# Kernel optimization log

Measured on AMD Instinct MI355X. Metric: run time of the kernel, lower is better.

The kernel has to match this reference:

```python
import jax, jax.numpy as jnp
import numpy as np

B, N = 1, 512
CS, CZ = 384, 128
H, DQK, DV, PQK, PV = 12, 16, 16, 4, 8
EPS = 1e-8
SW = float(np.sqrt(1.0 / (3 * DQK)))            # scalar_weights
PW = float(np.sqrt(1.0 / (3 * PQK * 9.0 / 2)))  # point_weights
ZW = float(np.sqrt(1.0 / 3))                    # attention_2d_weights


def _lin(key, din, dout):
    return 0.02 * jax.random.normal(key, (din, dout), dtype=jnp.float32), jnp.zeros((dout,), dtype=jnp.float32)


def setup_inputs():
    key = jax.random.key(0)
    ks = jax.random.split(key, 16)
    Wsq, bsq = _lin(ks[0], CS, H * DQK)
    Wsk, bsk = _lin(ks[1], CS, H * DQK)
    Wsv, bsv = _lin(ks[2], CS, H * DV)
    Wsb, bsb = _lin(ks[3], CZ, H)
    Wpq, bpq = _lin(ks[4], CS, H * PQK * 3)
    Wpk, bpk = _lin(ks[5], CS, H * PQK * 3)
    Wpv, bpv = _lin(ks[6], CS, H * PV * 3)
    Wout, bout = _lin(ks[7], H * (DV + PV * 4 + CZ), CS)
    w_attn = 0.5 * jax.random.normal(ks[8], (3,), dtype=jnp.float32)  # attn_linear weight (1,3)
    b_attn = jnp.zeros((), dtype=jnp.float32)
    tpw = jnp.full((H,), float(np.log(np.e - 1.0)), dtype=jnp.float32)  # trainable_point_weight
    s = jax.random.normal(ks[9], (B, N, CS), dtype=jnp.float32)
    z = jax.random.normal(ks[10], (B, N, N, CZ), dtype=jnp.float32)
    rot = jax.random.normal(ks[11], (B, N, 3, 3), dtype=jnp.float32)
    tran = jax.random.normal(ks[12], (B, N, 3), dtype=jnp.float32)
    res_mask = jnp.ones((B, N), dtype=jnp.float32)
    return dict(s=s, z=z, rot=rot, tran=tran, res_mask=res_mask,
                Wsq=Wsq, bsq=bsq, Wsk=Wsk, bsk=bsk, Wsv=Wsv, bsv=bsv,
                Wsb=Wsb, bsb=bsb, Wpq=Wpq, bpq=bpq, Wpk=Wpk, bpk=bpk,
                Wpv=Wpv, bpv=bpv, w_attn=w_attn, b_attn=b_attn, tpw=tpw,
                Wout=Wout, bout=bout)


def _ipa(s, z, rot, tran, res_mask, Wsq, bsq, Wsk, bsk, Wsv, bsv, Wsb, bsb,
         Wpq, bpq, Wpk, bpk, Wpv, bpv, w_attn, b_attn, tpw, Wout, bout):
    b, n, _ = s.shape
    sq = (s @ Wsq + bsq).reshape(b, n, H, DQK)
    sk = (s @ Wsk + bsk).reshape(b, n, H, DQK)
    sv = (s @ Wsv + bsv).reshape(b, n, H, DV)
    sb = z @ Wsb + bsb  # [b, i, j, h] pair bias

    def to_global(W, bias, p):
        t = (s @ W + bias).reshape(b, n, H, p, 3)
        return jnp.einsum('bnxy,bnhpy->bnhpx', rot, t) + tran[:, :, None, None, :]

    pqg = to_global(Wpq, bpq, PQK)
    pkg = to_global(Wpk, bpk, PQK)
    pvg = to_global(Wpv, bpv, PV)

    diff = pqg[:, :, None] - pkg[:, None, :]          # [b, i, j, h, p, 3]
    sdist = jnp.sum(diff * diff, axis=(-1, -2))       # [b, i, j, h]

    attn_point = -0.5 * jax.nn.softplus(tpw) * sdist * PW
    attn_scalar = jnp.einsum('bihd,bjhd->bijh', sq * SW, sk)
    attn_pair = sb * ZW
    # attn_linear(stack([scalar, point, pair], -1)).squeeze(-1)
    logits = attn_scalar * w_attn[0] + attn_point * w_attn[1] + attn_pair * w_attn[2] + b_attn

    mask2d = res_mask[:, :, None] * res_mask[:, None, :]
    logits = jnp.where(mask2d[..., None] == 0, jnp.finfo(logits.dtype).min, logits)
    attn = jax.nn.softmax(logits, axis=2)             # softmax over j

    r_scalar = jnp.einsum('bijh,bjhd->bihd', attn, sv)
    r_pt_g = jnp.einsum('bijh,bjhpc->bihpc', attn, pvg)
    # rotate back to local frame: R^T (x - t)
    r_pt = jnp.einsum('biyx,bihpy->bihpx', rot, r_pt_g - tran[:, :, None, None, :])
    r_norm = jnp.sqrt(jnp.sum(r_pt * r_pt, axis=-1) + EPS)  # [b, i, h, p]
    r_pair = jnp.einsum('bijh,bijc->bihc', attn, z)

    cat = jnp.concatenate([r_scalar, r_pt.reshape(b, n, H, PV * 3), r_norm, r_pair], axis=-1)
    return cat.reshape(b, n, -1) @ Wout + bout


def reference(s, z, rot, tran, res_mask, Wsq, bsq, Wsk, bsk, Wsv, bsv, Wsb, bsb,
              Wpq, bpq, Wpk, bpk, Wpv, bpv, w_attn, b_attn, tpw, Wout, bout):
    return _ipa(s, z, rot, tran, res_mask, Wsq, bsq, Wsk, bsk, Wsv, bsv, Wsb, bsb,
                Wpq, bpq, Wpk, bpk, Wpv, bpv, w_attn, b_attn, tpw, Wout, bout)
```

## Files before the change

### kernel.cpp

```cpp
#include <hip/hip_runtime.h>
#include <hip/hip_bf16.h>
#include <math.h>

#define NN 512
#define CSD 384
#define CZ 128
#define HH 12
#define TMPW 1152
#define CATH 176
#define CATDIM 2112
#define NSPLIT 6
#define KSPL 352

#define SW 0.14433756729740643f
#define PW 0.13608276348795434f
#define ZW 0.57735026918962576f
#define NEG_INF -3.4028234663852886e38f

typedef float f32x4_t __attribute__((ext_vector_type(4)));
typedef short bf16x8_t __attribute__((ext_vector_type(8)));

union BFU { uint4 q; bf16x8_t v; ushort u[8]; };

static __device__ __forceinline__ ushort f2bf(float f) {
    __hip_bfloat16 h = __float2bfloat16(f);
    return *reinterpret_cast<ushort*>(&h);
}
static __device__ __forceinline__ float bf2f(ushort u) {
    unsigned int v = ((unsigned int)u) << 16;
    return __uint_as_float(v);
}

__global__ void proj_gemm_kernel(const float* __restrict__ s, const float* __restrict__ rot,
                                 const float* __restrict__ tran,
                                 const float* __restrict__ Wsq, const float* __restrict__ bsq,
                                 const float* __restrict__ Wsk, const float* __restrict__ bsk,
                                 const float* __restrict__ Wsv, const float* __restrict__ bsv,
                                 const float* __restrict__ Wpq, const float* __restrict__ bpq,
                                 const float* __restrict__ Wpk, const float* __restrict__ bpk,
                                 const float* __restrict__ Wpv, const float* __restrict__ bpv,
                                 float* __restrict__ tmp)
{
    int bx = blockIdx.x;
    int n0 = blockIdx.y * 32;
    int f0 = bx * 48;
    const float* W; const float* bb; int dout; int segstart;
    if (bx < 4)       { W = Wsq; bb = bsq; dout = 192; segstart = 0; }
    else if (bx < 8)  { W = Wsk; bb = bsk; dout = 192; segstart = 192; }
    else if (bx < 12) { W = Wsv; bb = bsv; dout = 192; segstart = 384; }
    else if (bx < 15) { W = Wpq; bb = bpq; dout = 144; segstart = 576; }
    else if (bx < 18) { W = Wpk; bb = bpk; dout = 144; segstart = 720; }
    else              { W = Wpv; bb = bpv; dout = 288; segstart = 864; }
    int colbase = f0 - segstart;

    __shared__ float St[32][34];
    __shared__ float Ws[32][49];
    int tid = threadIdx.x;
    int ty = tid >> 4, tx = tid & 15;
    float acc[2][3] = {{0,0,0},{0,0,0}};

    for (int k0 = 0; k0 < CSD; k0 += 32) {
        {
            int r = tid >> 3, c4 = (tid & 7) * 4;
            float4 v = *(const float4*)&s[(size_t)(n0 + r) * CSD + k0 + c4];
            St[c4 + 0][r] = v.x; St[c4 + 1][r] = v.y; St[c4 + 2][r] = v.z; St[c4 + 3][r] = v.w;
        }
        for (int e = tid; e < 1536; e += 256) {
            int r = e / 48, c = e % 48;
            Ws[r][c] = W[(size_t)(k0 + r) * dout + colbase + c];
        }
        __syncthreads();
        #pragma unroll
        for (int k = 0; k < 32; k++) {
            float2 a = *(const float2*)&St[k][ty * 2];
            float b0 = Ws[k][tx * 3], b1 = Ws[k][tx * 3 + 1], b2 = Ws[k][tx * 3 + 2];
            acc[0][0] += a.x * b0; acc[0][1] += a.x * b1; acc[0][2] += a.x * b2;
            acc[1][0] += a.y * b0; acc[1][1] += a.y * b1; acc[1][2] += a.y * b2;
        }
        __syncthreads();
    }
    float bv0 = bb[colbase + tx * 3], bv1 = bb[colbase + tx * 3 + 1], bv2 = bb[colbase + tx * 3 + 2];
    #pragma unroll
    for (int r = 0; r < 2; r++) {
        int n = n0 + ty * 2 + r;
        float v0 = acc[r][0] + bv0, v1 = acc[r][1] + bv1, v2 = acc[r][2] + bv2;
        float* o = tmp + (size_t)n * TMPW + f0 + tx * 3;
        if (bx >= 12) {
            const float* R = rot + n * 9;
            const float* T = tran + n * 3;
            float g0 = R[0] * v0 + R[1] * v1 + R[2] * v2 + T[0];
            float g1 = R[3] * v0 + R[4] * v1 + R[5] * v2 + T[1];
            float g2 = R[6] * v0 + R[7] * v1 + R[8] * v2 + T[2];
            o[0] = g0; o[1] = g1; o[2] = g2;
        } else {
            o[0] = v0; o[1] = v1; o[2] = v2;
        }
    }
}

__global__ __launch_bounds__(256) void logits_kernel(
        const float* __restrict__ z, const float* __restrict__ resm,
        const float* __restrict__ Wsb, const float* __restrict__ bsb,
        const float* __restrict__ watt, const float* __restrict__ batt,
        const float* __restrict__ tpw, const float* __restrict__ tmp,
        float* __restrict__ lgts)
{
    int jc = blockIdx.x;
    int i  = blockIdx.y;
    __shared__ float sqs[12 * 24];
    __shared__ float pqi[12 * 24];
    __shared__ float cpt[12];
    __shared__ float cb[12];
    int tid = threadIdx.x;
    int w = tid >> 6, lane = tid & 63;
    int l16 = lane & 15, lhi = lane >> 4;
    float w0 = watt[0], w1 = watt[1], w2 = watt[2], ba = batt[0];
    float A2 = w2 * ZW;

    if (tid < 192) {
        int h = tid >> 4, d = tid & 15;
        sqs[h * 24 + d] = tmp[(size_t)i * TMPW + tid] * (SW * w0);
    }
    if (tid < 144) {
        int h = tid / 12, d = tid % 12;
        pqi[h * 24 + d] = tmp[(size_t)i * TMPW + 576 + tid];
    }
    if (tid < 12) {
        cpt[tid] = -0.5f * log1pf(expf(tpw[tid])) * PW * w1;
        cb[tid]  = A2 * bsb[tid] + ba;
    }

    BFU breg[4];
    #pragma unroll
    for (int kk = 0; kk < 4; kk++) {
        #pragma unroll
        for (int e = 0; e < 8; e++) {
            int k = kk * 32 + lhi * 8 + e;
            float v = (l16 < HH) ? Wsb[k * HH + l16] * A2 : 0.f;
            breg[kk].u[e] = f2bf(v);
        }
    }
    __syncthreads();

    const float* zi = z + (size_t)i * NN * CZ;
    float rmi = resm[i];
    float cpth = cpt[l16 < HH ? l16 : 0];
    float cbh  = cb[l16 < HH ? l16 : 0];

    #pragma unroll
    for (int t = 0; t < 2; t++) {
        int jbase = jc * 128 + (w * 2 + t) * 16;
        const float* zr = zi + (size_t)(jbase + l16) * CZ + lhi * 8;
        float4 pr[8];
        #pragma unroll
        for (int kk = 0; kk < 4; kk++) {
            pr[kk * 2]     = *(const float4*)&zr[kk * 32];
            pr[kk * 2 + 1] = *(const float4*)&zr[kk * 32 + 4];
        }
        f32x4_t acc = {0.f, 0.f, 0.f, 0.f};
        #pragma unroll
        for (int kk = 0; kk < 4; kk++) {
            float4 f0 = pr[kk * 2], f1 = pr[kk * 2 + 1];
            BFU a;
            a.u[0] = f2bf(f0.x); a.u[1] = f2bf(f0.y); a.u[2] = f2bf(f0.z); a.u[3] = f2bf(f0.w);
            a.u[4] = f2bf(f1.x); a.u[5] = f2bf(f1.y); a.u[6] = f2bf(f1.z); a.u[7] = f2bf(f1.w);
            acc = __builtin_amdgcn_mfma_f32_16x16x32_bf16(a.v, breg[kk].v, acc, 0, 0, 0);
        }
        if (l16 < HH) {
            int h = l16;
            const float4* sqp = (const float4*)&sqs[h * 24];
            const float4* pqp = (const float4*)&pqi[h * 24];
            #pragma unroll
            for (int r = 0; r < 4; r++) {
                int j = jbase + lhi * 4 + r;
                float mj = rmi * resm[j];
                const float4* skp = (const float4*)(tmp + (size_t)j * TMPW + 192 + h * 16);
                float d0 = 0.f;
                #pragma unroll
                for (int q = 0; q < 4; q++) {
                    float4 kv = skp[q];
                    float4 qv = sqp[q];
                    d0 += qv.x * kv.x + qv.y * kv.y + qv.z * kv.z + qv.w * kv.w;
                }
                const float4* pkp = (const float4*)(tmp + (size_t)j * TMPW + 720 + h * 12);
                float sd = 0.f;
                #pragma unroll
                for (int q = 0; q < 3; q++) {
                    float4 kv = pkp[q];
                    float4 qv = pqp[q];
                    float a = qv.x - kv.x, bb2 = qv.y - kv.y, cc = qv.z - kv.z, e = qv.w - kv.w;
                    sd += a * a + bb2 * bb2 + cc * cc + e * e;
                }
                float lg = cbh + acc[r] + d0 + cpth * sd;
                if (mj == 0.f) lg = NEG_INF;
                lgts[((size_t)i * HH + h) * NN + j] = lg;
            }
        }
    }
}

__global__ __launch_bounds__(256) void softmax_kernel(const float* __restrict__ lgts,
                                                      ushort* __restrict__ attn_bf)
{
    int tid = threadIdx.x;
    int w = tid >> 6, lane = tid & 63;
    int gid = blockIdx.x * 4 + w;
    const float* row = lgts + (size_t)gid * NN;
    float v[8]; float m = -INFINITY;
    #pragma unroll
    for (int u = 0; u < 8; u++) { v[u] = row[lane + 64 * u]; m = fmaxf(m, v[u]); }
    for (int off = 32; off; off >>= 1) m = fmaxf(m, __shfl_xor(m, off));
    float ssum = 0.f;
    #pragma unroll
    for (int u = 0; u < 8; u++) { v[u] = __expf(v[u] - m); ssum += v[u]; }
    for (int off = 32; off; off >>= 1) ssum += __shfl_xor(ssum, off);
    float inv = 1.f / ssum;
    ushort* ag = attn_bf + (size_t)gid * NN;
    #pragma unroll
    for (int u = 0; u < 8; u++) ag[lane + 64 * u] = f2bf(v[u] * inv);
}

__global__ __launch_bounds__(256) void rpair_kernel(const float* __restrict__ z,
                                                    const ushort* __restrict__ attn_bf,
                                                    float* __restrict__ part)
{
    int jq = blockIdx.x;
    int i  = blockIdx.y;
    __shared__ ushort pbf[128 * 12];
    __shared__ float pslab[4 * 12 * 128];
    int tid = threadIdx.x;

    if (tid < 192) {
        int h = tid >> 4, g = tid & 15;
        BFU v; v.q = *(const uint4*)&attn_bf[((size_t)i * HH + h) * NN + jq * 128 + g * 8];
        #pragma unroll
        for (int q = 0; q < 8; q++) pbf[(g * 8 + q) * 12 + h] = v.u[q];
    }
    __syncthreads();

    int w = tid >> 6, lane = tid & 63;
    int c0 = lane * 2;
    const float* zq = z + ((size_t)i * NN + jq * 128 + w * 32) * CZ + c0;
    float acc[12][2];
    #pragma unroll
    for (int h = 0; h < 12; h++) { acc[h][0] = 0.f; acc[h][1] = 0.f; }

    for (int j0 = 0; j0 < 32; j0 += 8) {
        float2 zv[8];
        #pragma unroll
        for (int u = 0; u < 8; u++) zv[u] = *(const float2*)&zq[(size_t)(j0 + u) * CZ];
        #pragma unroll
        for (int u = 0; u < 8; u++) {
            int jl = w * 32 + j0 + u;
            const uint2* pr = (const uint2*)&pbf[jl * 12];
            uint2 pa = pr[0], pb2 = pr[1], pc = pr[2];
            float ph[12];
            ph[0]  = bf2f((ushort)(pa.x & 0xffff)); ph[1]  = bf2f((ushort)(pa.x >> 16));
            ph[2]  = bf2f((ushort)(pa.y & 0xffff)); ph[3]  = bf2f((ushort)(pa.y >> 16));
            ph[4]  = bf2f((ushort)(pb2.x & 0xffff)); ph[5]  = bf2f((ushort)(pb2.x >> 16));
            ph[6]  = bf2f((ushort)(pb2.y & 0xffff)); ph[7]  = bf2f((ushort)(pb2.y >> 16));
            ph[8]  = bf2f((ushort)(pc.x & 0xffff)); ph[9]  = bf2f((ushort)(pc.x >> 16));
            ph[10] = bf2f((ushort)(pc.y & 0xffff)); ph[11] = bf2f((ushort)(pc.y >> 16));
            #pragma unroll
            for (int h = 0; h < 12; h++) {
                acc[h][0] += ph[h] * zv[u].x;
                acc[h][1] += ph[h] * zv[u].y;
            }
        }
    }
    #pragma unroll
    for (int h = 0; h < 12; h++)
        *(float2*)&pslab[(w * 12 + h) * 128 + c0] = make_float2(acc[h][0], acc[h][1]);
    __syncthreads();

    for (int e = tid; e < 1536; e += 256) {
        float ssum = pslab[e] + pslab[1536 + e] + pslab[3072 + e] + pslab[4608 + e];
        part[((size_t)jq * NN + i) * 1536 + e] = ssum;
    }
}

__global__ void combine_rpair_kernel(const float* __restrict__ part, float* __restrict__ cat)
{
    int v = blockIdx.x * 256 + threadIdx.x;
    int i = v / 1536, hc = v % 1536;
    int h = hc >> 7, c = hc & 127;
    float ssum = part[(size_t)i * 1536 + hc]
               + part[((size_t)NN + i) * 1536 + hc]
               + part[((size_t)2 * NN + i) * 1536 + hc]
               + part[((size_t)3 * NN + i) * 1536 + hc];
    cat[(size_t)i * CATDIM + h * CATH + 48 + c] = ssum;
}

__global__ void head_sum_kernel(const ushort* __restrict__ attn_bf, const float* __restrict__ tmp,
                                const float* __restrict__ rot, const float* __restrict__ tran,
                                float* __restrict__ cat)
{
    int i0 = blockIdx.x * 32;
    int h  = blockIdx.y;
    __shared__ float At[32][65];
    __shared__ float Sr[64][44];
    __shared__ float Rp[32][24];
    int tid = threadIdx.x;
    int il = tid & 31, fg = tid >> 5;
    float acc[5] = {0,0,0,0,0};

    for (int jc = 0; jc < NN; jc += 64) {
        {
            int r = tid >> 3, c8 = (tid & 7) * 8;
            const ushort* src = attn_bf + ((size_t)(i0 + r) * HH + h) * NN + jc + c8;
            BFU v; v.q = *(const uint4*)src;
            #pragma unroll
            for (int q = 0; q < 8; q++) At[r][c8 + q] = bf2f(v.u[q]);
        }
        {
            int jr = tid >> 2, d4 = (tid & 3) * 4;
            *(float4*)&Sr[jr][d4] = *(const float4*)&tmp[(size_t)(jc + jr) * TMPW + 384 + h * 16 + d4];
        }
        for (int e = tid; e < 384; e += 256) {
            int jr = e / 6, p4 = (e % 6) * 4;
            *(float4*)&Sr[jr][16 + p4] = *(const float4*)&tmp[(size_t)(jc + jr) * TMPW + 864 + h * 24 + p4];
        }
        __syncthreads();
        #pragma unroll 4
        for (int j = 0; j < 64; j++) {
            float a = At[il][j];
            #pragma unroll
            for (int q = 0; q < 5; q++) acc[q] += a * Sr[j][fg * 5 + q];
        }
        __syncthreads();
    }

    float* cbase = cat + (size_t)(i0 + il) * CATDIM + h * CATH;
    #pragma unroll
    for (int q = 0; q < 5; q++) {
        int f = fg * 5 + q;
        if (f < 16) cbase[f] = acc[q];
        else Rp[il][f - 16] = acc[q];
    }
    __syncthreads();

    {
        int il2 = tid >> 3, p = tid & 7;
        int i = i0 + il2;
        float gx = Rp[il2][p * 3 + 0] - tran[i * 3 + 0];
        float gy = Rp[il2][p * 3 + 1] - tran[i * 3 + 1];
        float gz = Rp[il2][p * 3 + 2] - tran[i * 3 + 2];
        const float* R = rot + i * 9;
        float lx = R[0] * gx + R[3] * gy + R[6] * gz;
        float ly = R[1] * gx + R[4] * gy + R[7] * gz;
        float lz = R[2] * gx + R[5] * gy + R[8] * gz;
        float nrm = sqrtf(lx * lx + ly * ly + lz * lz + 1e-8f);
        float* cp = cat + (size_t)i * CATDIM + h * CATH;
        cp[16 + p * 3 + 0] = lx; cp[16 + p * 3 + 1] = ly; cp[16 + p * 3 + 2] = lz;
        cp[40 + p] = nrm;
    }
}

__global__ void out_gemm_split_kernel(const float* __restrict__ cat, const float* __restrict__ Wout,
                                      float* __restrict__ part)
{
    int n0 = blockIdx.x * 64;
    int i0 = blockIdx.y * 64;
    int ks = blockIdx.z * KSPL;
    __shared__ float St[32][68];
    __shared__ float Bs[32][68];
    int tid = threadIdx.x;
    int ty = tid >> 4, tx = tid & 15;
    float acc[4][4] = {{0,0,0,0},{0,0,0,0},{0,0,0,0},{0,0,0,0}};

    for (int k0 = 0; k0 < KSPL; k0 += 32) {
        {
            int r = tid >> 2, c8 = (tid & 3) * 8;
            const float* src = cat + (size_t)(i0 + r) * CATDIM + ks + k0 + c8;
            float4 v0 = *(const float4*)src;
            float4 v1 = *(const float4*)(src + 4);
            St[c8+0][r]=v0.x; St[c8+1][r]=v0.y; St[c8+2][r]=v0.z; St[c8+3][r]=v0.w;
            St[c8+4][r]=v1.x; St[c8+5][r]=v1.y; St[c8+6][r]=v1.z; St[c8+7][r]=v1.w;
        }
        {
            int r = tid >> 3, c8 = (tid & 7) * 8;
            const float* src = Wout + (size_t)(ks + k0 + r) * CSD + n0 + c8;
            *(float4*)&Bs[r][c8]     = *(const float4*)src;
            *(float4*)&Bs[r][c8 + 4] = *(const float4*)(src + 4);
        }
        __syncthreads();
        #pragma unroll
        for (int k = 0; k < 32; k++) {
            float4 a = *(const float4*)&St[k][ty * 4];
            float4 b = *(const float4*)&Bs[k][tx * 4];
            float av[4] = {a.x, a.y, a.z, a.w};
            float bv[4] = {b.x, b.y, b.z, b.w};
            #pragma unroll
            for (int r = 0; r < 4; r++)
                #pragma unroll
                for (int c = 0; c < 4; c++) acc[r][c] += av[r] * bv[c];
        }
        __syncthreads();
    }
    #pragma unroll
    for (int r = 0; r < 4; r++) {
        float4 v = make_float4(acc[r][0], acc[r][1], acc[r][2], acc[r][3]);
        *(float4*)&part[((size_t)blockIdx.z * NN + i0 + ty * 4 + r) * CSD + n0 + tx * 4] = v;
    }
}

__global__ void reduce_out_kernel(const float* __restrict__ part, const float* __restrict__ bout,
                                  float* __restrict__ out)
{
    int v = blockIdx.x * 256 + threadIdx.x;
    int n4 = v % 96;
    float4 o = ((const float4*)bout)[n4];
    const float4* p4 = (const float4*)part;
    #pragma unroll
    for (int s = 0; s < NSPLIT; s++) {
        float4 t = p4[(size_t)s * 49152 + v];
        o.x += t.x; o.y += t.y; o.z += t.z; o.w += t.w;
    }
    ((float4*)out)[v] = o;
}

extern "C" void kernel_launch(void* const* d_in, const int* in_sizes, int n_in,
                              void* d_out, int out_size, void* d_ws, size_t ws_size,
                              hipStream_t stream) {
    const float* s    = (const float*)d_in[0];
    const float* z    = (const float*)d_in[1];
    const float* rot  = (const float*)d_in[2];
    const float* tran = (const float*)d_in[3];
    const float* resm = (const float*)d_in[4];
    const float* Wsq  = (const float*)d_in[5];  const float* bsq = (const float*)d_in[6];
    const float* Wsk  = (const float*)d_in[7];  const float* bsk = (const float*)d_in[8];
    const float* Wsv  = (const float*)d_in[9];  const float* bsv = (const float*)d_in[10];
    const float* Wsb  = (const float*)d_in[11]; const float* bsb = (const float*)d_in[12];
    const float* Wpq  = (const float*)d_in[13]; const float* bpq = (const float*)d_in[14];
    const float* Wpk  = (const float*)d_in[15]; const float* bpk = (const float*)d_in[16];
    const float* Wpv  = (const float*)d_in[17]; const float* bpv = (const float*)d_in[18];
    const float* watt = (const float*)d_in[19]; const float* batt = (const float*)d_in[20];
    const float* tpw  = (const float*)d_in[21];
    const float* Wout = (const float*)d_in[22]; const float* bout = (const float*)d_in[23];
    float* out = (float*)d_out;
    float* ws  = (float*)d_ws;

    float*  tmp     = ws;
    ushort* attn_bf = (ushort*)(ws + 589824);
    float*  lgts    = ws + 589824 + 1572864;
    float*  partR   = lgts + 3145728;
    float*  cat     = partR + 3145728;
    float*  partO   = cat + 1081344;

    proj_gemm_kernel<<<dim3(24, 16), 256, 0, stream>>>(s, rot, tran,
                                                       Wsq, bsq, Wsk, bsk, Wsv, bsv,
                                                       Wpq, bpq, Wpk, bpk, Wpv, bpv, tmp);
    logits_kernel<<<dim3(4, 512), 256, 0, stream>>>(z, resm, Wsb, bsb, watt, batt,
                                                    tpw, tmp, lgts);
    softmax_kernel<<<1536, 256, 0, stream>>>(lgts, attn_bf);
    rpair_kernel<<<dim3(4, 512), 256, 0, stream>>>(z, attn_bf, partR);
    combine_rpair_kernel<<<3072, 256, 0, stream>>>(partR, cat);
    head_sum_kernel<<<dim3(16, 12), 256, 0, stream>>>(attn_bf, tmp, rot, tran, cat);
    out_gemm_split_kernel<<<dim3(6, 8, NSPLIT), 256, 0, stream>>>(cat, Wout, partO);
    reduce_out_kernel<<<192, 256, 0, stream>>>(partO, bout, out);
}
```

Before: 200.5 us.

## Compute scalar and point logits as augmented bf16 MFMA GEMM fused into softmax

The squared point distance is expanded algebraically into q·k plus norm terms, so the scalar, point and bias logit contributions become one 32-wide augmented dot product. A prep kernel builds bf16 Q/K augmented matrices, and the softmax kernel computes the 16x512 tile per head with MFMA before adding the z-derived logits. The z-logits kernel now only does the pair-bias MFMA, dropping the per-element fp32 gathers from tmp. The rpair loop is also unrolled to 16 z loads in flight. Rounding the operands to bf16 and cancellation in the expanded distance (|q|²+|k|²-2q·k) can reduce logit accuracy, and the change adds one extra launch.

```diff
diff --git a/kernel.cpp b/kernel.cpp
--- a/kernel.cpp
+++ b/kernel.cpp
@@ -98,37 +98,66 @@
     }
 }
 
-__global__ __launch_bounds__(256) void logits_kernel(
-        const float* __restrict__ z, const float* __restrict__ resm,
-        const float* __restrict__ Wsb, const float* __restrict__ bsb,
-        const float* __restrict__ watt, const float* __restrict__ batt,
-        const float* __restrict__ tpw, const float* __restrict__ tmp,
-        float* __restrict__ lgts)
+__global__ void augprep_kernel(const float* __restrict__ tmp,
+                               const float* __restrict__ watt, const float* __restrict__ batt,
+                               const float* __restrict__ tpw, const float* __restrict__ bsb,
+                               ushort* __restrict__ Qaug, ushort* __restrict__ Kaug)
+{
+    int n = blockIdx.x;
+    int tid = threadIdx.x;
+    float w0 = watt[0], w1 = watt[1], w2 = watt[2], ba = batt[0];
+    float A2 = w2 * ZW;
+    __shared__ float nq[12], nk[12];
+    if (tid < 24) {
+        int h = tid >> 1, which = tid & 1;
+        const float* p = tmp + (size_t)n * TMPW + (which ? 720 : 576) + h * 12;
+        float s2 = 0.f;
+        #pragma unroll
+        for (int d = 0; d < 12; d++) s2 += p[d] * p[d];
+        if (which) nk[h] = s2; else nq[h] = s2;
+    }
+    __syncthreads();
+
+    for (int f = tid; f < 384; f += 256) {
+        if (f < 192) {
+            int h = f >> 4, k = f & 15;
+            float sq = tmp[(size_t)n * TMPW + h * 16 + k] * (SW * w0);
+            float sk = tmp[(size_t)n * TMPW + 192 + h * 16 + k];
+            Qaug[((size_t)h * NN + n) * 32 + k] = f2bf(sq);
+            Kaug[((size_t)h * NN + n) * 32 + k] = f2bf(sk);
+        } else if (f < 336) {
+            int e = f - 192; int h = e / 12, d = e % 12;
+            float cpt = -0.5f * log1pf(expf(tpw[h])) * PW * w1;
+            float pq = tmp[(size_t)n * TMPW + 576 + h * 12 + d];
+            float pk = tmp[(size_t)n * TMPW + 720 + h * 12 + d];
+            Qaug[((size_t)h * NN + n) * 32 + 16 + d] = f2bf(-2.f * cpt * pq);
+            Kaug[((size_t)h * NN + n) * 32 + 16 + d] = f2bf(pk);
+        } else {
+            int e = f - 336; int h = e >> 2, sl = e & 3;
+            float cpt = -0.5f * log1pf(expf(tpw[h])) * PW * w1;
+            float qv, kv;
+            if (sl == 0)      { qv = cpt * nq[h];      kv = 1.f; }
+            else if (sl == 1) { qv = cpt;              kv = nk[h]; }
+            else if (sl == 2) { qv = A2 * bsb[h] + ba; kv = 1.f; }
+            else              { qv = 0.f;              kv = 0.f; }
+            Qaug[((size_t)h * NN + n) * 32 + 28 + sl] = f2bf(qv);
+            Kaug[((size_t)h * NN + n) * 32 + 28 + sl] = f2bf(kv);
+        }
+    }
+}
+
+__global__ __launch_bounds__(256) void zlogits_kernel(const float* __restrict__ z,
+                                                      const float* __restrict__ resm,
+                                                      const float* __restrict__ Wsb,
+                                                      const float* __restrict__ watt,
+                                                      float* __restrict__ lgts)
 {
     int jc = blockIdx.x;
     int i  = blockIdx.y;
-    __shared__ float sqs[12 * 24];
-    __shared__ float pqi[12 * 24];
-    __shared__ float cpt[12];
-    __shared__ float cb[12];
     int tid = threadIdx.x;
     int w = tid >> 6, lane = tid & 63;
     int l16 = lane & 15, lhi = lane >> 4;
-    float w0 = watt[0], w1 = watt[1], w2 = watt[2], ba = batt[0];
-    float A2 = w2 * ZW;
-
-    if (tid < 192) {
-        int h = tid >> 4, d = tid & 15;
-        sqs[h * 24 + d] = tmp[(size_t)i * TMPW + tid] * (SW * w0);
-    }
-    if (tid < 144) {
-        int h = tid / 12, d = tid % 12;
-        pqi[h * 24 + d] = tmp[(size_t)i * TMPW + 576 + tid];
-    }
-    if (tid < 12) {
-        cpt[tid] = -0.5f * log1pf(expf(tpw[tid])) * PW * w1;
-        cb[tid]  = A2 * bsb[tid] + ba;
-    }
+    float A2 = watt[2] * ZW;
 
     BFU breg[4];
     #pragma unroll
@@ -140,12 +169,9 @@
             breg[kk].u[e] = f2bf(v);
         }
     }
-    __syncthreads();
 
     const float* zi = z + (size_t)i * NN * CZ;
     float rmi = resm[i];
-    float cpth = cpt[l16 < HH ? l16 : 0];
-    float cbh  = cb[l16 < HH ? l16 : 0];
 
     #pragma unroll
     for (int t = 0; t < 2; t++) {
@@ -167,57 +193,63 @@
             acc = __builtin_amdgcn_mfma_f32_16x16x32_bf16(a.v, breg[kk].v, acc, 0, 0, 0);
         }
         if (l16 < HH) {
-            int h = l16;
-            const float4* sqp = (const float4*)&sqs[h * 24];
-            const float4* pqp = (const float4*)&pqi[h * 24];
             #pragma unroll
             for (int r = 0; r < 4; r++) {
                 int j = jbase + lhi * 4 + r;
                 float mj = rmi * resm[j];
-                const float4* skp = (const float4*)(tmp + (size_t)j * TMPW + 192 + h * 16);
-                float d0 = 0.f;
-                #pragma unroll
-                for (int q = 0; q < 4; q++) {
-                    float4 kv = skp[q];
-                    float4 qv = sqp[q];
-                    d0 += qv.x * kv.x + qv.y * kv.y + qv.z * kv.z + qv.w * kv.w;
-                }
-                const float4* pkp = (const float4*)(tmp + (size_t)j * TMPW + 720 + h * 12);
-                float sd = 0.f;
-                #pragma unroll
-                for (int q = 0; q < 3; q++) {
-                    float4 kv = pkp[q];
-                    float4 qv = pqp[q];
-                    float a = qv.x - kv.x, bb2 = qv.y - kv.y, cc = qv.z - kv.z, e = qv.w - kv.w;
-                    sd += a * a + bb2 * bb2 + cc * cc + e * e;
-                }
-                float lg = cbh + acc[r] + d0 + cpth * sd;
+                float lg = acc[r];
                 if (mj == 0.f) lg = NEG_INF;
-                lgts[((size_t)i * HH + h) * NN + j] = lg;
+                lgts[((size_t)i * HH + l16) * NN + j] = lg;
             }
         }
     }
 }
 
-__global__ __launch_bounds__(256) void softmax_kernel(const float* __restrict__ lgts,
-                                                      ushort* __restrict__ attn_bf)
-{
+__global__ __launch_bounds__(256) void augsm_kernel(const float* __restrict__ lgts,
+                                                    const ushort* __restrict__ Qaug,
+                                                    const ushort* __restrict__ Kaug,
+                                                    ushort* __restrict__ attn_bf)
+{
+    int it = blockIdx.x;
+    int h  = blockIdx.y;
+    __shared__ float Dt[16][520];
     int tid = threadIdx.x;
     int w = tid >> 6, lane = tid & 63;
-    int gid = blockIdx.x * 4 + w;
-    const float* row = lgts + (size_t)gid * NN;
-    float v[8]; float m = -INFINITY;
-    #pragma unroll
-    for (int u = 0; u < 8; u++) { v[u] = row[lane + 64 * u]; m = fmaxf(m, v[u]); }
-    for (int off = 32; off; off >>= 1) m = fmaxf(m, __shfl_xor(m, off));
-    float ssum = 0.f;
-    #pragma unroll
-    for (int u = 0; u < 8; u++) { v[u] = __expf(v[u] - m); ssum += v[u]; }
-    for (int off = 32; off; off >>= 1) ssum += __shfl_xor(ssum, off);
-    float inv = 1.f / ssum;
-    ushort* ag = attn_bf + (size_t)gid * NN;
-    #pragma unroll
-    for (int u = 0; u < 8; u++) ag[lane + 64 * u] = f2bf(v[u] * inv);
+    int l16 = lane & 15, lhi = lane >> 4;
+
+    BFU a;
+    a.q = *(const uint4*)&Qaug[(((size_t)h * NN) + it * 16 + l16) * 32 + lhi * 8];
+
+    for (int jt = w; jt < 32; jt += 4) {
+        BFU b;
+        b.q = *(const uint4*)&Kaug[(((size_t)h * NN) + jt * 16 + l16) * 32 + lhi * 8];
+        f32x4_t acc = {0.f, 0.f, 0.f, 0.f};
+        acc = __builtin_amdgcn_mfma_f32_16x16x32_bf16(a.v, b.v, acc, 0, 0, 0);
+        #pragma unroll
+        for (int r = 0; r < 4; r++) Dt[lhi * 4 + r][jt * 16 + l16] = acc[r];
+    }
+    __syncthreads();
+
+    #pragma unroll
+    for (int rr = 0; rr < 4; rr++) {
+        int row = w * 4 + rr;
+        const float* lrow = lgts + (((size_t)(it * 16 + row)) * HH + h) * NN;
+        float v[8]; float m = -INFINITY;
+        #pragma unroll
+        for (int u = 0; u < 8; u++) {
+            v[u] = lrow[lane + 64 * u] + Dt[row][lane + 64 * u];
+            m = fmaxf(m, v[u]);
+        }
+        for (int off = 32; off; off >>= 1) m = fmaxf(m, __shfl_xor(m, off));
+        float ssum = 0.f;
+        #pragma unroll
+        for (int u = 0; u < 8; u++) { v[u] = __expf(v[u] - m); ssum += v[u]; }
+        for (int off = 32; off; off >>= 1) ssum += __shfl_xor(ssum, off);
+        float inv = 1.f / ssum;
+        ushort* ag = attn_bf + (((size_t)(it * 16 + row)) * HH + h) * NN;
+        #pragma unroll
+        for (int u = 0; u < 8; u++) ag[lane + 64 * u] = f2bf(v[u] * inv);
+    }
 }
 
 __global__ __launch_bounds__(256) void rpair_kernel(const float* __restrict__ z,
@@ -245,12 +277,13 @@
     #pragma unroll
     for (int h = 0; h < 12; h++) { acc[h][0] = 0.f; acc[h][1] = 0.f; }
 
-    for (int j0 = 0; j0 < 32; j0 += 8) {
-        float2 zv[8];
-        #pragma unroll
-        for (int u = 0; u < 8; u++) zv[u] = *(const float2*)&zq[(size_t)(j0 + u) * CZ];
-        #pragma unroll
-        for (int u = 0; u < 8; u++) {
+    #pragma unroll
+    for (int j0 = 0; j0 < 32; j0 += 16) {
+        float2 zv[16];
+        #pragma unroll
+        for (int u = 0; u < 16; u++) zv[u] = *(const float2*)&zq[(size_t)(j0 + u) * CZ];
+        #pragma unroll
+        for (int u = 0; u < 16; u++) {
             int jl = w * 32 + j0 + u;
             const uint2* pr = (const uint2*)&pbf[jl * 12];
             uint2 pa = pr[0], pb2 = pr[1], pc = pr[2];
@@ -442,17 +475,19 @@
 
     float*  tmp     = ws;
     ushort* attn_bf = (ushort*)(ws + 589824);
-    float*  lgts    = ws + 589824 + 1572864;
-    float*  partR   = lgts + 3145728;
-    float*  cat     = partR + 3145728;
-    float*  partO   = cat + 1081344;
+    float*  lgts    = ws + 2162688;
+    float*  partR   = ws + 5308416;
+    ushort* Qaug    = (ushort*)(ws + 8454144);
+    ushort* Kaug    = (ushort*)(ws + 8552448);
+    float*  cat     = ws + 8650752;
+    float*  partO   = ws + 9732096;
 
     proj_gemm_kernel<<<dim3(24, 16), 256, 0, stream>>>(s, rot, tran,
                                                        Wsq, bsq, Wsk, bsk, Wsv, bsv,
                                                        Wpq, bpq, Wpk, bpk, Wpv, bpv, tmp);
-    logits_kernel<<<dim3(4, 512), 256, 0, stream>>>(z, resm, Wsb, bsb, watt, batt,
-                                                    tpw, tmp, lgts);
-    softmax_kernel<<<1536, 256, 0, stream>>>(lgts, attn_bf);
+    augprep_kernel<<<512, 256, 0, stream>>>(tmp, watt, batt, tpw, bsb, Qaug, Kaug);
+    zlogits_kernel<<<dim3(4, 512), 256, 0, stream>>>(z, resm, Wsb, watt, lgts);
+    augsm_kernel<<<dim3(32, 12), 256, 0, stream>>>(lgts, Qaug, Kaug, attn_bf);
     rpair_kernel<<<dim3(4, 512), 256, 0, stream>>>(z, attn_bf, partR);
     combine_rpair_kernel<<<3072, 256, 0, stream>>>(partR, cat);
     head_sum_kernel<<<dim3(16, 12), 256, 0, stream>>>(attn_bf, tmp, rot, tran, cat);
```

Result: faster. 184.3 us (-8.0%).
